# Kernel optimization log

Hardware: AMD Instinct MI355X
Metric: run time of the kernel (lower is better)

## Reference

```python
import jax, jax.numpy as jnp
import numpy as np

D_OUT = 1024

def setup_inputs() -> dict:
    key = jax.random.key(0)
    k1, k2, k3, k4 = jax.random.split(key, 4)
    x = jax.random.normal(k1, (4, 2048, 1024), dtype=jnp.float32)
    # torch.nn.Linear weights are [d_out, d_in]
    s = 1.0 / np.sqrt(1024)
    W_q = jax.random.uniform(k2, (D_OUT, 1024), dtype=jnp.float32, minval=-s, maxval=s)
    W_k = jax.random.uniform(k3, (D_OUT, 1024), dtype=jnp.float32, minval=-s, maxval=s)
    W_v = jax.random.uniform(k4, (D_OUT, 1024), dtype=jnp.float32, minval=-s, maxval=s)
    return {"x": x, "W_q": W_q, "W_k": W_k, "W_v": W_v}

def reference(x, W_q, W_k, W_v):
    b, n, d_in = x.shape
    q = jnp.einsum('bnd,od->bno', x, W_q)  # [b, n, d_out]
    k = jnp.einsum('bnd,od->bno', x, W_k)
    v = jnp.einsum('bnd,od->bno', x, W_v)
    scores = jnp.einsum('bqd,bkd->bqk', q, k)  # full N x N score matrix
    causal = jnp.tril(jnp.ones((n, n), dtype=bool))
    scores = jnp.where(causal, scores, -jnp.inf)
    weights = jax.nn.softmax(scores / jnp.sqrt(jnp.float32(D_OUT)), axis=-1)
    # dropout p=0.0 -> identity (eval)
    return jnp.einsum('bqk,bkd->bqd', weights, v)
```

## Files before the change

kernel.cpp:

```cpp
#include <hip/hip_runtime.h>
#include <hip/hip_bf16.h>
#include <stdint.h>

typedef unsigned short ushort_t;
typedef __attribute__((ext_vector_type(4))) float f32x4;
typedef __attribute__((ext_vector_type(8))) __bf16 bf16x8;
typedef __attribute__((ext_vector_type(8))) unsigned short ushort8;
typedef __attribute__((ext_vector_type(4))) unsigned short ushort4v;

__device__ __forceinline__ float bf2f(ushort_t u) {
  union { unsigned u32; float f; } x; x.u32 = ((unsigned)u) << 16; return x.f;
}
__device__ __forceinline__ ushort_t f2bf(float f) {
  union { float f; unsigned u; } x; x.f = f;
  unsigned r = x.u + 0x7FFF + ((x.u >> 16) & 1);
  return (ushort_t)(r >> 16);
}

__device__ __forceinline__ void gld16(const ushort_t* g, ushort_t* l) {
  __builtin_amdgcn_global_load_lds(
      (const __attribute__((address_space(1))) uint32_t*)g,
      (__attribute__((address_space(3))) uint32_t*)l, 16, 0, 0);
}

__global__ __launch_bounds__(256) void cast_all_kernel(
    const float* __restrict__ x, const float* __restrict__ wq,
    const float* __restrict__ wk, const float* __restrict__ wv,
    ushort_t* __restrict__ xb, ushort_t* __restrict__ wqb,
    ushort_t* __restrict__ wkb, ushort_t* __restrict__ wvb,
    float* __restrict__ rowsum) {
  int blk = blockIdx.x;
  if (blk >= 4096 + 1536) {
    int idx = (blk - (4096 + 1536)) * 256 + threadIdx.x;
    f32x4 z = {0.f, 0.f, 0.f, 0.f};
    ((f32x4*)rowsum)[idx * 2] = z;
    ((f32x4*)rowsum)[idx * 2 + 1] = z;
    return;
  }
  const float* in;
  ushort_t* out;
  int i;
  if (blk < 4096) {
    in = x; out = xb; i = blk * 256 + threadIdx.x;
  } else {
    int w = (blk - 4096) >> 9;
    int lb = (blk - 4096) & 511;
    in = (w == 0) ? wq : (w == 1) ? wk : wv;
    out = (w == 0) ? wqb : (w == 1) ? wkb : wvb;
    i = lb * 256 + threadIdx.x;
  }
  const f32x4* p = (const f32x4*)in;
  f32x4 a = p[2 * i];
  f32x4 b = p[2 * i + 1];
  ushort8 o;
  o[0] = f2bf(a[0]); o[1] = f2bf(a[1]); o[2] = f2bf(a[2]); o[3] = f2bf(a[3]);
  o[4] = f2bf(b[0]); o[5] = f2bf(b[1]); o[6] = f2bf(b[2]); o[7] = f2bf(b[3]);
  *((ushort8*)out + i) = o;
}

#define BM 128
#define BN 128
#define BK 64

enum { OUT_EXP = 0, OUT_F32N = 2 };

__device__ __forceinline__ void gemm_core(
    const ushort_t* __restrict__ A, const ushort_t* __restrict__ B, int Kd,
    int kEnd, int m0, int n0, ushort_t* As, ushort_t* Bs, f32x4 (&acc)[4][4]) {
  int tid = threadIdx.x;
  int lane = tid & 63;
  int wave = tid >> 6;
  int wr = (wave >> 1) * 64;
  int wc = (wave & 1) * 64;
  int ln15 = lane & 15;
  int kq = lane >> 4;

  int row = tid >> 3;
  int ksw = ((tid & 7) ^ (row & 7)) * 8;
  const ushort_t* aB = A + (size_t)(m0 + row) * Kd + ksw;
  const ushort_t* bB = B + (size_t)(n0 + row) * Kd + ksw;
  int xk = ln15 & 7;

  for (int k0 = 0; k0 < kEnd; k0 += BK) {
    __syncthreads();
#pragma unroll
    for (int r = 0; r < 4; ++r) {
      gld16(aB + (size_t)(32 * r) * Kd + k0, &As[(tid + 256 * r) * 8]);
      gld16(bB + (size_t)(32 * r) * Kd + k0, &Bs[(tid + 256 * r) * 8]);
    }
    __syncthreads();
#pragma unroll
    for (int s = 0; s < 2; ++s) {
      bf16x8 af[4], bfr[4];
#pragma unroll
      for (int i = 0; i < 4; ++i)
        af[i] = *(const bf16x8*)
            &As[(wr + i * 16 + ln15) * BK + (((s * 4 + kq) ^ xk) * 8)];
#pragma unroll
      for (int j = 0; j < 4; ++j)
        bfr[j] = *(const bf16x8*)
            &Bs[(wc + j * 16 + ln15) * BK + (((s * 4 + kq) ^ xk) * 8)];
#pragma unroll
      for (int i = 0; i < 4; ++i)
#pragma unroll
        for (int j = 0; j < 4; ++j)
          acc[i][j] = __builtin_amdgcn_mfma_f32_16x16x32_bf16(
              af[i], bfr[j], acc[i][j], 0, 0, 0);
    }
  }
}

template <int OUT, bool CAUSAL_SKIP, bool K_LIMIT, bool REV_M>
__global__ __launch_bounds__(256, 3) void gemm_bt(
    const ushort_t* __restrict__ Ag, const ushort_t* __restrict__ Bg,
    void* __restrict__ Cg, int N, int Kd,
    long sA, long sB, long sC, float scale, float* __restrict__ rowsum) {
  int mIdx = REV_M ? (gridDim.x - 1 - blockIdx.x) : blockIdx.x;
  int m0 = mIdx * BM, n0 = blockIdx.y * BN;
  if (CAUSAL_SKIP && n0 > m0 + (BM - 1)) return;
  int bz = blockIdx.z;
  const ushort_t* A = Ag + (size_t)bz * sA;
  const ushort_t* B = Bg + (size_t)bz * sB;
  int kEnd = K_LIMIT ? min(Kd, m0 + BM) : Kd;

  __shared__ ushort_t As[BM * BK];
  __shared__ ushort_t Bs[BN * BK];

  f32x4 acc[4][4];
#pragma unroll
  for (int i = 0; i < 4; ++i)
#pragma unroll
    for (int j = 0; j < 4; ++j) acc[i][j] = f32x4{0.f, 0.f, 0.f, 0.f};

  gemm_core(A, B, Kd, kEnd, m0, n0, As, Bs, acc);

  int tid = threadIdx.x;
  int lane = tid & 63;
  int wave = tid >> 6;
  int wr = (wave >> 1) * 64;
  int wc = (wave & 1) * 64;
  int ln15 = lane & 15;
  int kq = lane >> 4;

  if (OUT == OUT_EXP) {
    ushort_t* C = (ushort_t*)Cg + (size_t)bz * sC;
    float* rs = rowsum + (size_t)bz * 2048;
#pragma unroll
    for (int i = 0; i < 4; ++i) {
      int row0 = m0 + wr + i * 16 + kq * 4;
#pragma unroll
      for (int r = 0; r < 4; ++r) {
        int grow = row0 + r;
        float psum = 0.f;
#pragma unroll
        for (int j = 0; j < 4; ++j) {
          int col = n0 + wc + j * 16 + ln15;
          float e = (col <= grow) ? __expf(acc[i][j][r] * scale) : 0.f;
          C[(size_t)grow * N + col] = f2bf(e);
          psum += e;
        }
        psum += __shfl_xor(psum, 1);
        psum += __shfl_xor(psum, 2);
        psum += __shfl_xor(psum, 4);
        psum += __shfl_xor(psum, 8);
        if (ln15 == 0) atomicAdd(&rs[grow], psum);
      }
    }
  } else {
    float* C = (float*)Cg + (size_t)bz * sC;
    const float* rs = rowsum + (size_t)bz * 2048;
#pragma unroll
    for (int i = 0; i < 4; ++i) {
      int row0 = m0 + wr + i * 16 + kq * 4;
#pragma unroll
      for (int r = 0; r < 4; ++r) {
        float inv = 1.0f / rs[row0 + r];
#pragma unroll
        for (int j = 0; j < 4; ++j) {
          int col = n0 + wc + j * 16 + ln15;
          C[(size_t)(row0 + r) * N + col] = acc[i][j][r] * inv;
        }
      }
    }
  }
}

__global__ __launch_bounds__(256, 3) void gemm_qkv(
    const ushort_t* __restrict__ xb, const ushort_t* __restrict__ wq,
    const ushort_t* __restrict__ wk, const ushort_t* __restrict__ wv,
    ushort_t* __restrict__ Qb, ushort_t* __restrict__ Kb,
    ushort_t* __restrict__ Vt) {
  int m0 = blockIdx.x * BM, n0 = blockIdx.y * BN;
  int z = blockIdx.z;
  const ushort_t* B = (z == 0) ? wq : (z == 1) ? wk : wv;

  __shared__ ushort_t As[BM * BK];
  __shared__ ushort_t Bs[BN * BK];

  f32x4 acc[4][4];
#pragma unroll
  for (int i = 0; i < 4; ++i)
#pragma unroll
    for (int j = 0; j < 4; ++j) acc[i][j] = f32x4{0.f, 0.f, 0.f, 0.f};

  gemm_core(xb, B, 1024, 1024, m0, n0, As, Bs, acc);

  int tid = threadIdx.x;
  int lane = tid & 63;
  int wave = tid >> 6;
  int wr = (wave >> 1) * 64;
  int wc = (wave & 1) * 64;
  int ln15 = lane & 15;
  int kq = lane >> 4;

  if (z < 2) {
    ushort_t* C = (z == 0) ? Qb : Kb;
#pragma unroll
    for (int i = 0; i < 4; ++i) {
      int row0 = m0 + wr + i * 16 + kq * 4;
#pragma unroll
      for (int j = 0; j < 4; ++j) {
        int col = n0 + wc + j * 16 + ln15;
#pragma unroll
        for (int r = 0; r < 4; ++r)
          C[(size_t)(row0 + r) * 1024 + col] = f2bf(acc[i][j][r]);
      }
    }
  } else {
#pragma unroll
    for (int i = 0; i < 4; ++i) {
      int gm = m0 + wr + i * 16 + kq * 4;
      int b = gm >> 11, nn = gm & 2047;
#pragma unroll
      for (int j = 0; j < 4; ++j) {
        int d = n0 + wc + j * 16 + ln15;
        ushort4v v;
#pragma unroll
        for (int r = 0; r < 4; ++r) v[r] = f2bf(acc[i][j][r]);
        *(ushort4v*)&Vt[(size_t)b * (2048 * 1024) + (size_t)d * 2048 + nn] = v;
      }
    }
  }
}

extern "C" void kernel_launch(void* const* d_in, const int* in_sizes, int n_in,
                              void* d_out, int out_size, void* d_ws, size_t ws_size,
                              hipStream_t stream) {
  const float* x = (const float*)d_in[0];
  const float* Wq = (const float*)d_in[1];
  const float* Wk = (const float*)d_in[2];
  const float* Wv = (const float*)d_in[3];
  float* out = (float*)d_out;
  char* ws = (char*)d_ws;

  ushort_t* xb = (ushort_t*)(ws);
  ushort_t* wqb = (ushort_t*)(ws + (16ull << 20));
  ushort_t* wkb = (ushort_t*)(ws + (18ull << 20));
  ushort_t* wvb = (ushort_t*)(ws + (20ull << 20));
  ushort_t* Qb = (ushort_t*)(ws + (22ull << 20));
  ushort_t* Kb = (ushort_t*)(ws + (38ull << 20));
  ushort_t* Vt = (ushort_t*)(ws + (54ull << 20));
  ushort_t* Eb = (ushort_t*)(ws + (70ull << 20));
  float* rowsum = (float*)(ws + (102ull << 20));

  cast_all_kernel<<<4096 + 3 * 512 + 4, 256, 0, stream>>>(
      x, Wq, Wk, Wv, xb, wqb, wkb, wvb, rowsum);

  dim3 gQKV(8192 / BM, 1024 / BN, 3);
  gemm_qkv<<<gQKV, 256, 0, stream>>>(xb, wqb, wkb, wvb, Qb, Kb, Vt);

  dim3 gS(2048 / BM, 2048 / BN, 4);
  gemm_bt<OUT_EXP, true, false, false><<<gS, 256, 0, stream>>>(
      Qb, Kb, Eb, 2048, 1024, 2048 * 1024, 2048 * 1024, 2048 * 2048,
      0.03125f, rowsum);

  dim3 gO(2048 / BM, 1024 / BN, 4);
  gemm_bt<OUT_F32N, false, true, true><<<gO, 256, 0, stream>>>(
      Eb, Vt, out, 1024, 2048, 2048 * 2048, 1024 * 2048, 2048 * 1024,
      1.0f, rowsum);
}
```

Baseline: 223.1 us.

## Switch GEMMs to 8-wave 256x128 tiles with triple-buffered LDS prefetch pipeline

Replaces the single-buffered 128x128 GEMM core with an 8-wave (512-thread) 256x128 tile core. It uses three LDS stages, loads two K-tiles ahead, and splits each K step into two MFMA phases with barriers and raised priority. The goal is to overlap global-to-LDS loads with MFMA work and cut the two full syncs per K step. It uses much more LDS per block (144KB), which limits occupancy, and causal-skip granularity becomes coarser. The reversed-M ordering for the output GEMM is dropped.

```diff
diff --git a/kernel.cpp b/kernel.cpp
--- a/kernel.cpp
+++ b/kernel.cpp
@@ -58,73 +58,191 @@
   *((ushort8*)out + i) = o;
 }
 
-#define BM 128
-#define BN 128
-#define BK 64
-
 enum { OUT_EXP = 0, OUT_F32N = 2 };
 
-__device__ __forceinline__ void gemm_core(
+__device__ __forceinline__ void gemm8_core(
     const ushort_t* __restrict__ A, const ushort_t* __restrict__ B, int Kd,
-    int kEnd, int m0, int n0, ushort_t* As, ushort_t* Bs, f32x4 (&acc)[4][4]) {
+    int kEnd, int m0, int n0,
+    ushort_t* a0, ushort_t* a1, ushort_t* a2,
+    ushort_t* b0, ushort_t* b1, ushort_t* b2,
+    f32x4 (&acc)[4][4]) {
   int tid = threadIdx.x;
   int lane = tid & 63;
   int wave = tid >> 6;
-  int wr = (wave >> 1) * 64;
-  int wc = (wave & 1) * 64;
+  int wm = wave >> 1;
+  int wn = wave & 1;
   int ln15 = lane & 15;
   int kq = lane >> 4;
-
-  int row = tid >> 3;
-  int ksw = ((tid & 7) ^ (row & 7)) * 8;
-  const ushort_t* aB = A + (size_t)(m0 + row) * Kd + ksw;
-  const ushort_t* bB = B + (size_t)(n0 + row) * Kd + ksw;
   int xk = ln15 & 7;
 
-  for (int k0 = 0; k0 < kEnd; k0 += BK) {
-    __syncthreads();
-#pragma unroll
-    for (int r = 0; r < 4; ++r) {
-      gld16(aB + (size_t)(32 * r) * Kd + k0, &As[(tid + 256 * r) * 8]);
-      gld16(bB + (size_t)(32 * r) * Kd + k0, &Bs[(tid + 256 * r) * 8]);
-    }
-    __syncthreads();
-#pragma unroll
-    for (int s = 0; s < 2; ++s) {
-      bf16x8 af[4], bfr[4];
-#pragma unroll
-      for (int i = 0; i < 4; ++i)
-        af[i] = *(const bf16x8*)
-            &As[(wr + i * 16 + ln15) * BK + (((s * 4 + kq) ^ xk) * 8)];
-#pragma unroll
-      for (int j = 0; j < 4; ++j)
-        bfr[j] = *(const bf16x8*)
-            &Bs[(wc + j * 16 + ln15) * BK + (((s * 4 + kq) ^ xk) * 8)];
-#pragma unroll
-      for (int i = 0; i < 4; ++i)
+  int rowc = tid >> 3;
+  int ksw = ((tid & 7) ^ (rowc & 7)) * 8;
+  const ushort_t* aB = A + (size_t)(m0 + rowc) * Kd + ksw;
+  const ushort_t* bB = B + (size_t)(n0 + rowc) * Kd + ksw;
+
+  const int nt = kEnd >> 6;
+
+  ushort_t *pAr = a0, *pAn = a1, *pAw = a2;
+  ushort_t *pBr = b0, *pBn = b1, *pBw = b2;
+
+#pragma unroll
+  for (int c = 0; c < 4; ++c)
+    gld16(aB + (size_t)(64 * c) * Kd, a0 + (size_t)(tid + 512 * c) * 8);
+#pragma unroll
+  for (int c = 0; c < 2; ++c)
+    gld16(bB + (size_t)(64 * c) * Kd, b0 + (size_t)(tid + 512 * c) * 8);
+#pragma unroll
+  for (int c = 0; c < 4; ++c)
+    gld16(aB + (size_t)(64 * c) * Kd + 64, a1 + (size_t)(tid + 512 * c) * 8);
+#pragma unroll
+  for (int c = 0; c < 2; ++c)
+    gld16(bB + (size_t)(64 * c) * Kd + 64, b1 + (size_t)(tid + 512 * c) * 8);
+  asm volatile("s_waitcnt vmcnt(6)" ::: "memory");
+  __builtin_amdgcn_s_barrier();
+
+  bf16x8 bfr[2][4];
+  for (int t = 0; t < nt; ++t) {
+    const bool st = (t + 2) < nt;
+    const int k2 = (t + 2) << 6;
+    bf16x8 af[2][2];
+#pragma unroll
+    for (int il = 0; il < 2; ++il) {
+      int ro = (wm * 64 + il * 16 + ln15) * 64;
+#pragma unroll
+      for (int s = 0; s < 2; ++s)
+        af[s][il] = *(const bf16x8*)&pAr[ro + (((s * 4 + kq) ^ xk) * 8)];
+    }
+#pragma unroll
+    for (int j = 0; j < 4; ++j) {
+      int ro = (wn * 64 + j * 16 + ln15) * 64;
+#pragma unroll
+      for (int s = 0; s < 2; ++s)
+        bfr[s][j] = *(const bf16x8*)&pBr[ro + (((s * 4 + kq) ^ xk) * 8)];
+    }
+    if (st) {
+      gld16(aB + (size_t)0 * Kd + k2, pAw + (size_t)tid * 8);
+      gld16(aB + (size_t)64 * Kd + k2, pAw + (size_t)(tid + 512) * 8);
+      gld16(bB + k2, pBw + (size_t)tid * 8);
+    }
+    __builtin_amdgcn_s_barrier();
+    asm volatile("s_waitcnt lgkmcnt(0)" ::: "memory");
+    __builtin_amdgcn_sched_barrier(0);
+    __builtin_amdgcn_s_setprio(1);
+#pragma unroll
+    for (int s = 0; s < 2; ++s)
+#pragma unroll
+      for (int il = 0; il < 2; ++il)
 #pragma unroll
         for (int j = 0; j < 4; ++j)
-          acc[i][j] = __builtin_amdgcn_mfma_f32_16x16x32_bf16(
-              af[i], bfr[j], acc[i][j], 0, 0, 0);
-    }
-  }
-}
-
-template <int OUT, bool CAUSAL_SKIP, bool K_LIMIT, bool REV_M>
-__global__ __launch_bounds__(256, 3) void gemm_bt(
+          acc[il][j] = __builtin_amdgcn_mfma_f32_16x16x32_bf16(
+              af[s][il], bfr[s][j], acc[il][j], 0, 0, 0);
+    __builtin_amdgcn_s_setprio(0);
+    __builtin_amdgcn_s_barrier();
+#pragma unroll
+    for (int il = 0; il < 2; ++il) {
+      int ro = (wm * 64 + (il + 2) * 16 + ln15) * 64;
+#pragma unroll
+      for (int s = 0; s < 2; ++s)
+        af[s][il] = *(const bf16x8*)&pAr[ro + (((s * 4 + kq) ^ xk) * 8)];
+    }
+    if (st) {
+      gld16(aB + (size_t)128 * Kd + k2, pAw + (size_t)(tid + 1024) * 8);
+      gld16(aB + (size_t)192 * Kd + k2, pAw + (size_t)(tid + 1536) * 8);
+      gld16(bB + (size_t)64 * Kd + k2, pBw + (size_t)(tid + 512) * 8);
+      asm volatile("s_waitcnt vmcnt(6)" ::: "memory");
+    } else {
+      asm volatile("s_waitcnt vmcnt(0)" ::: "memory");
+    }
+    __builtin_amdgcn_s_barrier();
+    asm volatile("s_waitcnt lgkmcnt(0)" ::: "memory");
+    __builtin_amdgcn_sched_barrier(0);
+    __builtin_amdgcn_s_setprio(1);
+#pragma unroll
+    for (int s = 0; s < 2; ++s)
+#pragma unroll
+      for (int il = 0; il < 2; ++il)
+#pragma unroll
+        for (int j = 0; j < 4; ++j)
+          acc[il + 2][j] = __builtin_amdgcn_mfma_f32_16x16x32_bf16(
+              af[s][il], bfr[s][j], acc[il + 2][j], 0, 0, 0);
+    __builtin_amdgcn_s_setprio(0);
+    __builtin_amdgcn_s_barrier();
+    ushort_t* tA = pAr; pAr = pAn; pAn = pAw; pAw = tA;
+    ushort_t* tB = pBr; pBr = pBn; pBn = pBw; pBw = tB;
+  }
+}
+
+__global__ __launch_bounds__(512, 2) void gemm_qkv8(
+    const ushort_t* __restrict__ xb, const ushort_t* __restrict__ wq,
+    const ushort_t* __restrict__ wk, const ushort_t* __restrict__ wv,
+    ushort_t* __restrict__ Qb, ushort_t* __restrict__ Kb,
+    ushort_t* __restrict__ Vt) {
+  int m0 = blockIdx.x * 256, n0 = blockIdx.y * 128;
+  int z = blockIdx.z;
+  const ushort_t* B = (z == 0) ? wq : (z == 1) ? wk : wv;
+
+  __shared__ ushort_t As[3][256 * 64];
+  __shared__ ushort_t Bs[3][128 * 64];
+
+  f32x4 acc[4][4];
+#pragma unroll
+  for (int i = 0; i < 4; ++i)
+#pragma unroll
+    for (int j = 0; j < 4; ++j) acc[i][j] = f32x4{0.f, 0.f, 0.f, 0.f};
+
+  gemm8_core(xb, B, 1024, 1024, m0, n0, As[0], As[1], As[2], Bs[0], Bs[1],
+             Bs[2], acc);
+
+  int tid = threadIdx.x;
+  int lane = tid & 63;
+  int wave = tid >> 6;
+  int wm = wave >> 1, wn = wave & 1;
+  int ln15 = lane & 15, kq = lane >> 4;
+
+  if (z < 2) {
+    ushort_t* C = (z == 0) ? Qb : Kb;
+#pragma unroll
+    for (int i = 0; i < 4; ++i) {
+      int row0 = m0 + wm * 64 + i * 16 + kq * 4;
+#pragma unroll
+      for (int j = 0; j < 4; ++j) {
+        int col = n0 + wn * 64 + j * 16 + ln15;
+#pragma unroll
+        for (int r = 0; r < 4; ++r)
+          C[(size_t)(row0 + r) * 1024 + col] = f2bf(acc[i][j][r]);
+      }
+    }
+  } else {
+#pragma unroll
+    for (int i = 0; i < 4; ++i) {
+      int gm = m0 + wm * 64 + i * 16 + kq * 4;
+      int b = gm >> 11, nn = gm & 2047;
+#pragma unroll
+      for (int j = 0; j < 4; ++j) {
+        int d = n0 + wn * 64 + j * 16 + ln15;
+        ushort4v v;
+#pragma unroll
+        for (int r = 0; r < 4; ++r) v[r] = f2bf(acc[i][j][r]);
+        *(ushort4v*)&Vt[(size_t)b * (2048 * 1024) + (size_t)d * 2048 + nn] = v;
+      }
+    }
+  }
+}
+
+template <int OUT, bool CAUSAL_SKIP, bool K_LIMIT>
+__global__ __launch_bounds__(512, 2) void gemm8k(
     const ushort_t* __restrict__ Ag, const ushort_t* __restrict__ Bg,
     void* __restrict__ Cg, int N, int Kd,
     long sA, long sB, long sC, float scale, float* __restrict__ rowsum) {
-  int mIdx = REV_M ? (gridDim.x - 1 - blockIdx.x) : blockIdx.x;
-  int m0 = mIdx * BM, n0 = blockIdx.y * BN;
-  if (CAUSAL_SKIP && n0 > m0 + (BM - 1)) return;
+  int m0 = blockIdx.x * 256, n0 = blockIdx.y * 128;
+  if (CAUSAL_SKIP && n0 > m0 + 255) return;
   int bz = blockIdx.z;
   const ushort_t* A = Ag + (size_t)bz * sA;
   const ushort_t* B = Bg + (size_t)bz * sB;
-  int kEnd = K_LIMIT ? min(Kd, m0 + BM) : Kd;
-
-  __shared__ ushort_t As[BM * BK];
-  __shared__ ushort_t Bs[BN * BK];
+  int kEnd = K_LIMIT ? min(Kd, m0 + 256) : Kd;
+
+  __shared__ ushort_t As[3][256 * 64];
+  __shared__ ushort_t Bs[3][128 * 64];
 
   f32x4 acc[4][4];
 #pragma unroll
@@ -132,29 +250,28 @@
 #pragma unroll
     for (int j = 0; j < 4; ++j) acc[i][j] = f32x4{0.f, 0.f, 0.f, 0.f};
 
-  gemm_core(A, B, Kd, kEnd, m0, n0, As, Bs, acc);
+  gemm8_core(A, B, Kd, kEnd, m0, n0, As[0], As[1], As[2], Bs[0], Bs[1], Bs[2],
+             acc);
 
   int tid = threadIdx.x;
   int lane = tid & 63;
   int wave = tid >> 6;
-  int wr = (wave >> 1) * 64;
-  int wc = (wave & 1) * 64;
-  int ln15 = lane & 15;
-  int kq = lane >> 4;
+  int wm = wave >> 1, wn = wave & 1;
+  int ln15 = lane & 15, kq = lane >> 4;
 
   if (OUT == OUT_EXP) {
     ushort_t* C = (ushort_t*)Cg + (size_t)bz * sC;
     float* rs = rowsum + (size_t)bz * 2048;
 #pragma unroll
     for (int i = 0; i < 4; ++i) {
-      int row0 = m0 + wr + i * 16 + kq * 4;
+      int row0 = m0 + wm * 64 + i * 16 + kq * 4;
 #pragma unroll
       for (int r = 0; r < 4; ++r) {
         int grow = row0 + r;
         float psum = 0.f;
 #pragma unroll
         for (int j = 0; j < 4; ++j) {
-          int col = n0 + wc + j * 16 + ln15;
+          int col = n0 + wn * 64 + j * 16 + ln15;
           float e = (col <= grow) ? __expf(acc[i][j][r] * scale) : 0.f;
           C[(size_t)grow * N + col] = f2bf(e);
           psum += e;
@@ -171,73 +288,15 @@
     const float* rs = rowsum + (size_t)bz * 2048;
 #pragma unroll
     for (int i = 0; i < 4; ++i) {
-      int row0 = m0 + wr + i * 16 + kq * 4;
+      int row0 = m0 + wm * 64 + i * 16 + kq * 4;
 #pragma unroll
       for (int r = 0; r < 4; ++r) {
         float inv = 1.0f / rs[row0 + r];
 #pragma unroll
         for (int j = 0; j < 4; ++j) {
-          int col = n0 + wc + j * 16 + ln15;
+          int col = n0 + wn * 64 + j * 16 + ln15;
           C[(size_t)(row0 + r) * N + col] = acc[i][j][r] * inv;
         }
-      }
-    }
-  }
-}
-
-__global__ __launch_bounds__(256, 3) void gemm_qkv(
-    const ushort_t* __restrict__ xb, const ushort_t* __restrict__ wq,
-    const ushort_t* __restrict__ wk, const ushort_t* __restrict__ wv,
-    ushort_t* __restrict__ Qb, ushort_t* __restrict__ Kb,
-    ushort_t* __restrict__ Vt) {
-  int m0 = blockIdx.x * BM, n0 = blockIdx.y * BN;
-  int z = blockIdx.z;
-  const ushort_t* B = (z == 0) ? wq : (z == 1) ? wk : wv;
-
-  __shared__ ushort_t As[BM * BK];
-  __shared__ ushort_t Bs[BN * BK];
-
-  f32x4 acc[4][4];
-#pragma unroll
-  for (int i = 0; i < 4; ++i)
-#pragma unroll
-    for (int j = 0; j < 4; ++j) acc[i][j] = f32x4{0.f, 0.f, 0.f, 0.f};
-
-  gemm_core(xb, B, 1024, 1024, m0, n0, As, Bs, acc);
-
-  int tid = threadIdx.x;
-  int lane = tid & 63;
-  int wave = tid >> 6;
-  int wr = (wave >> 1) * 64;
-  int wc = (wave & 1) * 64;
-  int ln15 = lane & 15;
-  int kq = lane >> 4;
-
-  if (z < 2) {
-    ushort_t* C = (z == 0) ? Qb : Kb;
-#pragma unroll
-    for (int i = 0; i < 4; ++i) {
-      int row0 = m0 + wr + i * 16 + kq * 4;
-#pragma unroll
-      for (int j = 0; j < 4; ++j) {
-        int col = n0 + wc + j * 16 + ln15;
-#pragma unroll
-        for (int r = 0; r < 4; ++r)
-          C[(size_t)(row0 + r) * 1024 + col] = f2bf(acc[i][j][r]);
-      }
-    }
-  } else {
-#pragma unroll
-    for (int i = 0; i < 4; ++i) {
-      int gm = m0 + wr + i * 16 + kq * 4;
-      int b = gm >> 11, nn = gm & 2047;
-#pragma unroll
-      for (int j = 0; j < 4; ++j) {
-        int d = n0 + wc + j * 16 + ln15;
-        ushort4v v;
-#pragma unroll
-        for (int r = 0; r < 4; ++r) v[r] = f2bf(acc[i][j][r]);
-        *(ushort4v*)&Vt[(size_t)b * (2048 * 1024) + (size_t)d * 2048 + nn] = v;
       }
     }
   }
@@ -266,16 +325,16 @@
   cast_all_kernel<<<4096 + 3 * 512 + 4, 256, 0, stream>>>(
       x, Wq, Wk, Wv, xb, wqb, wkb, wvb, rowsum);
 
-  dim3 gQKV(8192 / BM, 1024 / BN, 3);
-  gemm_qkv<<<gQKV, 256, 0, stream>>>(xb, wqb, wkb, wvb, Qb, Kb, Vt);
-
-  dim3 gS(2048 / BM, 2048 / BN, 4);
-  gemm_bt<OUT_EXP, true, false, false><<<gS, 256, 0, stream>>>(
+  dim3 gQKV(8192 / 256, 1024 / 128, 3);
+  gemm_qkv8<<<gQKV, 512, 0, stream>>>(xb, wqb, wkb, wvb, Qb, Kb, Vt);
+
+  dim3 gS(2048 / 256, 2048 / 128, 4);
+  gemm8k<OUT_EXP, true, false><<<gS, 512, 0, stream>>>(
       Qb, Kb, Eb, 2048, 1024, 2048 * 1024, 2048 * 1024, 2048 * 2048,
       0.03125f, rowsum);
 
-  dim3 gO(2048 / BM, 1024 / BN, 4);
-  gemm_bt<OUT_F32N, false, true, true><<<gO, 256, 0, stream>>>(
+  dim3 gO(2048 / 256, 1024 / 128, 4);
+  gemm8k<OUT_F32N, false, true><<<gO, 512, 0, stream>>>(
       Eb, Vt, out, 1024, 2048, 2048 * 2048, 1024 * 2048, 2048 * 1024,
       1.0f, rowsum);
 }
```

After: 239.3 us. 1.07x slower.
